# Optimization experiments

Measured on AMD Instinct MI355X. Metric: run time of the kernel, lower is better.

## Reference

```python
import jax, jax.numpy as jnp
import numpy as np

N_NODES = 50000
N_EDGES = 500000
NEG_SLOPE = 0.2


def gat_layer(x, src, dst, W, a_src, a_dst, b, n):
    """PyG-style GATConv (add_self_loops=True, concat=True, eval mode).
    x: [N, F_in], W: [F_in, H*C], a_src/a_dst: [H, C], b: [H*C]."""
    H, C = a_src.shape
    h = (x @ W).reshape(-1, H, C)              # [N, H, C]
    loops = jnp.arange(n, dtype=src.dtype)
    s = jnp.concatenate([src, loops])          # self-loops appended
    d = jnp.concatenate([dst, loops])
    alpha_src = jnp.einsum('nhc,hc->nh', h, a_src)   # [N, H]
    alpha_dst = jnp.einsum('nhc,hc->nh', h, a_dst)
    e = jax.nn.leaky_relu(alpha_src[s] + alpha_dst[d], NEG_SLOPE)  # [E+N, H]
    m = jax.ops.segment_max(e, d, num_segments=n)    # segment softmax over dst
    w = jnp.exp(e - m[d])
    denom = jax.ops.segment_sum(w, d, num_segments=n)
    attn = w / (denom[d] + 1e-16)                    # [E+N, H]
    msg = h[s] * attn[:, :, None]                    # [E+N, H, C]
    out = jax.ops.segment_sum(msg, d, num_segments=n)  # [N, H, C]
    return out.reshape(n, H * C) + b


def setup_inputs() -> dict:
    key = jax.random.key(0)
    ks = jax.random.split(key, 20)
    F_in, Hd, Hh = 128, 64, 4
    g = lambda k, shp, fan: jax.random.normal(k, shp, jnp.float32) * (1.0 / np.sqrt(fan))
    inp = {
        'x': jax.random.normal(ks[0], (N_NODES, F_in), jnp.float32),
        'edge_index': jax.random.randint(ks[1], (2, N_EDGES), 0, N_NODES, jnp.int32),
        'W1': g(ks[2], (F_in, Hh * Hd), F_in),
        'a1s': g(ks[3], (Hh, Hd), Hd), 'a1d': g(ks[4], (Hh, Hd), Hd),
        'b1': jnp.zeros((Hh * Hd,), jnp.float32),
        'W2': g(ks[5], (Hh * Hd, Hh * Hd), Hh * Hd),
        'a2s': g(ks[6], (Hh, Hd), Hd), 'a2d': g(ks[7], (Hh, Hd), Hd),
        'b2': jnp.zeros((Hh * Hd,), jnp.float32),
        'W3': g(ks[8], (Hh * Hd, Hd), Hh * Hd),
        'a3s': g(ks[9], (1, Hd), Hd), 'a3d': g(ks[10], (1, Hd), Hd),
        'b3': jnp.zeros((Hd,), jnp.float32),
        'cW1': g(ks[11], (Hd, Hd // 2), Hd), 'cb1': jnp.zeros((Hd // 2,), jnp.float32),
        'cW2': g(ks[12], (Hd // 2, 2), Hd // 2), 'cb2': jnp.zeros((2,), jnp.float32),
    }
    return inp


def reference(x, edge_index, W1, a1s, a1d, b1, W2, a2s, a2d, b2,
              W3, a3s, a3d, b3, cW1, cb1, cW2, cb2):
    n = x.shape[0]
    src, dst = edge_index[0], edge_index[1]
    h = jax.nn.elu(gat_layer(x, src, dst, W1, a1s, a1d, b1, n))
    h = jax.nn.elu(gat_layer(h, src, dst, W2, a2s, a2d, b2, n))
    h = jax.nn.relu(gat_layer(h, src, dst, W3, a3s, a3d, b3, n))
    h = jax.nn.relu(h @ cW1 + cb1)
    logits = h @ cW2 + cb2
    return jax.nn.log_softmax(logits, axis=1)
```

## Files before the change

### kernel.cpp

```cpp
#include <hip/hip_runtime.h>
#include <hip/hip_fp16.h>

#define LRELU(v) ((v) > 0.f ? (v) : 0.2f * (v))

typedef _Float16 f16x8 __attribute__((ext_vector_type(8)));
typedef float f32x4 __attribute__((ext_vector_type(4)));

__device__ __forceinline__ f16x8 f16x8_zero() {
    f16x8 v;
#pragma unroll
    for (int j = 0; j < 8; ++j) v[j] = (_Float16)0.f;
    return v;
}

__global__ __launch_bounds__(256) void hist_kernel(const int* __restrict__ dst,
                                                   int* __restrict__ cnt, int E) {
    int e = blockIdx.x * 256 + threadIdx.x;
    if (e < E) atomicAdd(&cnt[dst[e]], 1);
}

__global__ __launch_bounds__(256) void scan_blk(const int* __restrict__ cnt,
                                                int* __restrict__ offv,
                                                int* __restrict__ bsum, int N) {
    __shared__ int sh[256];
    const int t = threadIdx.x;
    const int base = blockIdx.x * 1024 + t * 4;
    int v0 = (base + 0 < N) ? cnt[base + 0] : 0;
    int v1 = (base + 1 < N) ? cnt[base + 1] : 0;
    int v2 = (base + 2 < N) ? cnt[base + 2] : 0;
    int v3 = (base + 3 < N) ? cnt[base + 3] : 0;
    const int T = v0 + v1 + v2 + v3;
    sh[t] = T;
    __syncthreads();
    for (int o = 1; o < 256; o <<= 1) {
        int x = (t >= o) ? sh[t - o] : 0;
        __syncthreads();
        sh[t] += x;
        __syncthreads();
    }
    const int excl = sh[t] - T;
    if (t == 255) bsum[blockIdx.x] = sh[255];
    if (base + 0 < N) offv[base + 0] = excl;
    if (base + 1 < N) offv[base + 1] = excl + v0;
    if (base + 2 < N) offv[base + 2] = excl + v0 + v1;
    if (base + 3 < N) offv[base + 3] = excl + v0 + v1 + v2;
}

__global__ __launch_bounds__(64) void scan_top(int* __restrict__ bsum,
                                               int* __restrict__ offv,
                                               int NB, int N) {
    const int t = threadIdx.x;
    const int v = (t < NB) ? bsum[t] : 0;
    int incl = v;
#pragma unroll
    for (int o = 1; o < 64; o <<= 1) {
        int x = __shfl_up(incl, o);
        if (t >= o) incl += x;
    }
    if (t < NB) bsum[t] = incl - v;
    if (t == NB - 1) offv[N] = incl;
}

__global__ __launch_bounds__(256) void scan_add(int* __restrict__ offv,
                                                const int* __restrict__ bsum, int N) {
    const int base = blockIdx.x * 1024 + threadIdx.x * 4;
    const int add = bsum[blockIdx.x];
#pragma unroll
    for (int i = 0; i < 4; ++i)
        if (base + i < N) offv[base + i] += add;
}

__global__ __launch_bounds__(256) void fill_kernel(const int* __restrict__ dst,
                                                   const int* __restrict__ srcv,
                                                   const int* __restrict__ offv,
                                                   int* __restrict__ cur,
                                                   int* __restrict__ csrsrc, int E) {
    int e = blockIdx.x * 256 + threadIdx.x;
    if (e < E) {
        int d = dst[e];
        int p = atomicAdd(&cur[d], 1);
        csrsrc[offv[d] + p] = srcv[e];
    }
}

__global__ __launch_bounds__(256) void prep_w16(const float* __restrict__ W,
                                                _Float16* __restrict__ wt,
                                                int K, int Nn) {
    int idx = blockIdx.x * 256 + threadIdx.x;
    if (idx < K * Nn) {
        int k = idx / Nn, nn2 = idx - k * Nn;
        wt[(size_t)nn2 * K + k] = (_Float16)W[idx];
    }
}

__global__ __launch_bounds__(256) void cvt_f16(const float* __restrict__ in,
                                               _Float16* __restrict__ out, int n4) {
    int i = blockIdx.x * 256 + threadIdx.x;
    if (i < n4) {
        float4 v = *(const float4*)(in + (size_t)i * 4);
        _Float16 o[4] = {(_Float16)v.x, (_Float16)v.y, (_Float16)v.z, (_Float16)v.w};
        *(float2*)(out + (size_t)i * 4) = *(float2*)o;
    }
}

template <int WM, int WN, int K, int H>
__global__ __launch_bounds__(WM * WN * 64) void gemm_f16_fused(
    const _Float16* __restrict__ A, const _Float16* __restrict__ Wt,
    const float* __restrict__ a_s, const float* __restrict__ a_d,
    _Float16* __restrict__ hout, float* __restrict__ als,
    float* __restrict__ ald, int M, int Nn) {
    constexpr int BM = WM * 64;
    constexpr int T = WM * WN * 64;
    constexpr int CHUNKS = BM * 16;
    __shared__ f16x8 Atile[BM * 16];
    const int t = threadIdx.x;
    const int lane = t & 63;
    const int wv = t >> 6;
    const int wm = wv / WN, wn = wv % WN;
    const int m0 = blockIdx.x * BM;
    const int n0 = blockIdx.y * (WN * 64);
    const int l15 = lane & 15, lg = lane >> 4;

    f32x4 acc[4][4];
    const f32x4 zz = {0.f, 0.f, 0.f, 0.f};
#pragma unroll
    for (int mi = 0; mi < 4; ++mi)
#pragma unroll
        for (int ni = 0; ni < 4; ++ni) acc[mi][ni] = zz;

    for (int kc = 0; kc < K; kc += 128) {
        __syncthreads();
#pragma unroll
        for (int i = 0; i < CHUNKS / T; ++i) {
            const int c = i * T + t;
            const int row = c >> 4, cc = c & 15;
            const int gr = m0 + row;
            f16x8 v = (gr < M) ? *(const f16x8*)(A + (size_t)gr * K + kc + cc * 8)
                               : f16x8_zero();
            Atile[(row * 16 + cc) ^ (row & 7)] = v;
        }
        __syncthreads();
#pragma unroll
        for (int ks = 0; ks < 4; ++ks) {
            f16x8 af[4], bf[4];
#pragma unroll
            for (int mi = 0; mi < 4; ++mi) {
                const int row = wm * 64 + mi * 16 + l15;
                af[mi] = Atile[(row * 16 + ks * 4 + lg) ^ (row & 7)];
            }
#pragma unroll
            for (int ni = 0; ni < 4; ++ni) {
                const int col = n0 + wn * 64 + ni * 16 + l15;
                bf[ni] = *(const f16x8*)(Wt + (size_t)col * K + kc + ks * 32 + lg * 8);
            }
#pragma unroll
            for (int mi = 0; mi < 4; ++mi)
#pragma unroll
                for (int ni = 0; ni < 4; ++ni)
                    acc[mi][ni] = __builtin_amdgcn_mfma_f32_16x16x32_f16(
                        af[mi], bf[ni], acc[mi][ni], 0, 0, 0);
        }
    }
    const int head = (n0 + wn * 64) >> 6;
    float a4s[4], a4d[4];
#pragma unroll
    for (int ni = 0; ni < 4; ++ni) {
        a4s[ni] = a_s[head * 64 + ni * 16 + l15];
        a4d[ni] = a_d[head * 64 + ni * 16 + l15];
    }
#pragma unroll
    for (int mi = 0; mi < 4; ++mi)
#pragma unroll
        for (int j = 0; j < 4; ++j) {
            const int r = m0 + wm * 64 + mi * 16 + lg * 4 + j;
            if (r < M) {
                float s1 = 0.f, s2 = 0.f;
#pragma unroll
                for (int ni = 0; ni < 4; ++ni) {
                    const float v = acc[mi][ni][j];
                    s1 += v * a4s[ni];
                    s2 += v * a4d[ni];
                    hout[(size_t)r * Nn + n0 + wn * 64 + ni * 16 + l15] = (_Float16)v;
                }
#pragma unroll
                for (int o = 8; o; o >>= 1) {
                    s1 += __shfl_xor(s1, o);
                    s2 += __shfl_xor(s2, o);
                }
                if (l15 == 0) {
                    als[(size_t)r * H + head] = s1;
                    ald[(size_t)r * H + head] = s2;
                }
            }
        }
}

__device__ __forceinline__ float sel4(float4 v, int h) {
    float r = v.x;
    r = (h == 1) ? v.y : r;
    r = (h == 2) ? v.z : r;
    r = (h == 3) ? v.w : r;
    return r;
}

__global__ __launch_bounds__(64) void gat_agg_h4(
    const __half* __restrict__ hhf, const float4* __restrict__ als4,
    const float4* __restrict__ ald4, const int* __restrict__ csrsrc,
    const int* __restrict__ offv, const float* __restrict__ bias,
    __half* __restrict__ outh) {
    const int n = blockIdx.x;
    const int t = threadIdx.x;
    const int hh = t >> 4;
    __shared__ int sid[64];
    __shared__ float4 wsh[64];
    const int start = offv[n];
    const int deg = offv[n + 1] - start;
    const float4 ad = ald4[n];
    const float4 asf = als4[n];
    float4 ws4;
    ws4.x = __expf(LRELU(asf.x + ad.x));
    ws4.y = __expf(LRELU(asf.y + ad.y));
    ws4.z = __expf(LRELU(asf.z + ad.z));
    ws4.w = __expf(LRELU(asf.w + ad.w));
    const float wself = sel4(ws4, hh);
    float acc[4];
    {
        float2 raw = *(const float2*)(hhf + (size_t)n * 256 + t * 4);
        __half2 h0 = *(__half2*)&raw.x;
        __half2 h1 = *(__half2*)&raw.y;
        float2 a0 = __half22float2(h0), a1 = __half22float2(h1);
        acc[0] = a0.x * wself; acc[1] = a0.y * wself;
        acc[2] = a1.x * wself; acc[3] = a1.y * wself;
    }
    float dsum = wself;

    for (int base = 0; base < deg; base += 64) {
        const int nb = deg - base;
        int s = 0;
        float4 w4 = {0.f, 0.f, 0.f, 0.f};
        if (t < nb) {
            s = csrsrc[start + base + t];
            const float4 av = als4[s];
            w4.x = __expf(LRELU(av.x + ad.x));
            w4.y = __expf(LRELU(av.y + ad.y));
            w4.z = __expf(LRELU(av.z + ad.z));
            w4.w = __expf(LRELU(av.w + ad.w));
        }
        __syncthreads();
        sid[t] = s;
        wsh[t] = w4;
        __syncthreads();
        const int nbc = min(nb, 64);
        const float* wflat = (const float*)wsh;
        for (int i = 0; i < nbc; ++i) {
            const int s2 = sid[i];
            const float wvv = wflat[i * 4 + hh];
            float2 raw = *(const float2*)(hhf + (size_t)s2 * 256 + t * 4);
            __half2 h0 = *(__half2*)&raw.x;
            __half2 h1 = *(__half2*)&raw.y;
            float2 a0 = __half22float2(h0), a1 = __half22float2(h1);
            dsum += wvv;
            acc[0] += a0.x * wvv; acc[1] += a0.y * wvv;
            acc[2] += a1.x * wvv; acc[3] += a1.y * wvv;
        }
    }
    const float inv = 1.f / (dsum + 1e-16f);
    const float4 bv = *(const float4*)(bias + t * 4);
    float4 o4;
    o4.x = acc[0] * inv + bv.x;
    o4.y = acc[1] * inv + bv.y;
    o4.z = acc[2] * inv + bv.z;
    o4.w = acc[3] * inv + bv.w;
    o4.x = (o4.x > 0.f) ? o4.x : (__expf(o4.x) - 1.f);
    o4.y = (o4.y > 0.f) ? o4.y : (__expf(o4.y) - 1.f);
    o4.z = (o4.z > 0.f) ? o4.z : (__expf(o4.z) - 1.f);
    o4.w = (o4.w > 0.f) ? o4.w : (__expf(o4.w) - 1.f);
    __half2 p0 = __floats2half2_rn(o4.x, o4.y);
    __half2 p1 = __floats2half2_rn(o4.z, o4.w);
    float2 st;
    *(__half2*)&st.x = p0;
    *(__half2*)&st.y = p1;
    *(float2*)(outh + (size_t)n * 256 + t * 4) = st;
}

__global__ __launch_bounds__(64) void gat_agg_h1_cls(
    const __half* __restrict__ hhf, const float* __restrict__ als,
    const float* __restrict__ ald, const int* __restrict__ csrsrc,
    const int* __restrict__ offv, const float* __restrict__ bias,
    const float* __restrict__ cW1, const float* __restrict__ cb1,
    const float* __restrict__ cW2, const float* __restrict__ cb2,
    float* __restrict__ outp) {
    const int n = blockIdx.x;
    const int t = threadIdx.x;
    __shared__ int sid[64];
    __shared__ float wsh[64];
    __shared__ float xs[64];
    __shared__ float hid[32];
    __shared__ float lg[2];
    const int start = offv[n];
    const int deg = offv[n + 1] - start;
    const float ad = ald[n];
    const float wself = __expf(LRELU(als[n] + ad));
    float acc = __half2float(hhf[(size_t)n * 64 + t]) * wself;
    float dsum = wself;

    for (int base = 0; base < deg; base += 64) {
        const int nb = deg - base;
        int s = 0;
        float w = 0.f;
        if (t < nb) {
            s = csrsrc[start + base + t];
            w = __expf(LRELU(als[s] + ad));
        }
        __syncthreads();
        sid[t] = s;
        wsh[t] = w;
        __syncthreads();
        const int nbc = min(nb, 64);
        for (int i = 0; i < nbc; ++i) {
            const float wvv = wsh[i];
            dsum += wvv;
            acc += __half2float(hhf[(size_t)sid[i] * 64 + t]) * wvv;
        }
    }
    float val = acc / (dsum + 1e-16f) + bias[t];
    val = fmaxf(val, 0.f);
    __syncthreads();
    xs[t] = val;
    __syncthreads();
    if (t < 32) {
        float s = cb1[t];
#pragma unroll
        for (int c = 0; c < 64; ++c) s += xs[c] * cW1[c * 32 + t];
        hid[t] = fmaxf(s, 0.f);
    }
    __syncthreads();
    if (t < 2) {
        float s = cb2[t];
#pragma unroll
        for (int j = 0; j < 32; ++j) s += hid[j] * cW2[j * 2 + t];
        lg[t] = s;
    }
    __syncthreads();
    if (t == 0) {
        float a = lg[0], b = lg[1];
        float mm = fmaxf(a, b);
        float lse = mm + logf(__expf(a - mm) + __expf(b - mm));
        outp[(size_t)n * 2 + 0] = a - lse;
        outp[(size_t)n * 2 + 1] = b - lse;
    }
}

extern "C" void kernel_launch(void* const* d_in, const int* in_sizes, int n_in,
                              void* d_out, int out_size, void* d_ws, size_t ws_size,
                              hipStream_t stream) {
    const float* x   = (const float*)d_in[0];
    const int*   ei  = (const int*)d_in[1];
    const float* W1  = (const float*)d_in[2];
    const float* a1s = (const float*)d_in[3];
    const float* a1d = (const float*)d_in[4];
    const float* b1  = (const float*)d_in[5];
    const float* W2  = (const float*)d_in[6];
    const float* a2s = (const float*)d_in[7];
    const float* a2d = (const float*)d_in[8];
    const float* b2  = (const float*)d_in[9];
    const float* W3  = (const float*)d_in[10];
    const float* a3s = (const float*)d_in[11];
    const float* a3d = (const float*)d_in[12];
    const float* b3  = (const float*)d_in[13];
    const float* cW1 = (const float*)d_in[14];
    const float* cb1 = (const float*)d_in[15];
    const float* cW2 = (const float*)d_in[16];
    const float* cb2 = (const float*)d_in[17];

    const int N = in_sizes[0] / 128;
    const int E = in_sizes[1] / 2;
    const int* srcv = ei;
    const int* dstv = ei + E;

    char* p = (char*)d_ws;
    _Float16* slotA = (_Float16*)p; p += (size_t)N * 256 * 2;
    _Float16* slotB = (_Float16*)p; p += (size_t)N * 256 * 2;
    _Float16* slotC = (_Float16*)p; p += (size_t)N * 128 * 2;
    float* als = (float*)p; p += (size_t)N * 4 * 4;
    float* ald = (float*)p; p += (size_t)N * 4 * 4;
    int* cnt = (int*)p; p += (size_t)N * 4;
    int* offv = (int*)p; p += (size_t)(N + 4) * 4;
    int* csr = (int*)p; p += (size_t)E * 4;
    _Float16* Wt1 = (_Float16*)p; p += (size_t)128 * 256 * 2;
    _Float16* Wt2 = (_Float16*)p; p += (size_t)256 * 256 * 2;
    _Float16* Wt3 = (_Float16*)p; p += (size_t)256 * 64 * 2;
    int* bsum = (int*)p;

    prep_w16<<<(128 * 256 + 255) / 256, 256, 0, stream>>>(W1, Wt1, 128, 256);
    prep_w16<<<(256 * 256 + 255) / 256, 256, 0, stream>>>(W2, Wt2, 256, 256);
    prep_w16<<<(256 * 64 + 255) / 256, 256, 0, stream>>>(W3, Wt3, 256, 64);
    cvt_f16<<<(N * 128 / 4 + 255) / 256, 256, 0, stream>>>(x, slotC, N * 128 / 4);

    const int NB = (N + 1023) / 1024;
    hipMemsetAsync(cnt, 0, (size_t)N * sizeof(int), stream);
    hist_kernel<<<(E + 255) / 256, 256, 0, stream>>>(dstv, cnt, E);
    scan_blk<<<NB, 256, 0, stream>>>(cnt, offv, bsum, N);
    scan_top<<<1, 64, 0, stream>>>(bsum, offv, NB, N);
    scan_add<<<NB, 256, 0, stream>>>(offv, bsum, N);
    hipMemsetAsync(cnt, 0, (size_t)N * sizeof(int), stream);
    fill_kernel<<<(E + 255) / 256, 256, 0, stream>>>(dstv, srcv, offv, cnt, csr, E);

    const int MB128 = (N + 127) / 128;
    const int MB256 = (N + 255) / 256;

    gemm_f16_fused<2, 4, 128, 4><<<dim3(MB128, 1), 512, 0, stream>>>(
        slotC, Wt1, a1s, a1d, slotA, als, ald, N, 256);
    gat_agg_h4<<<N, 64, 0, stream>>>((const __half*)slotA, (const float4*)als,
                                     (const float4*)ald, csr, offv, b1,
                                     (__half*)slotB);

    gemm_f16_fused<2, 4, 256, 4><<<dim3(MB128, 1), 512, 0, stream>>>(
        slotB, Wt2, a2s, a2d, slotA, als, ald, N, 256);
    gat_agg_h4<<<N, 64, 0, stream>>>((const __half*)slotA, (const float4*)als,
                                     (const float4*)ald, csr, offv, b2,
                                     (__half*)slotB);

    gemm_f16_fused<4, 1, 256, 1><<<dim3(MB256, 1), 256, 0, stream>>>(
        slotB, Wt3, a3s, a3d, slotA, als, ald, N, 64);
    gat_agg_h1_cls<<<N, 64, 0, stream>>>((const __half*)slotA, als, ald, csr, offv,
                                         b3, cW1, cb1, cW2, cb2, (float*)d_out);
}
```

Measured before the change: 296.0 us.

## Replace shared-memory staging with wave shuffles and pack four nodes per block

The aggregation kernels now process one destination node per 64-lane wavefront, with four nodes per 256-thread block. Edge indices and attention weights are broadcast with __shfl instead of being staged in LDS behind __syncthreads. The classifier head also uses shuffles rather than shared memory. In the 4-head kernel each 16-lane group computes its own head's weights for batches of 16 edges, which removes the per-block barriers and the tiny 64-thread blocks but means four times as many edge-batch iterations.

```diff
diff --git a/kernel.cpp b/kernel.cpp
--- a/kernel.cpp
+++ b/kernel.cpp
@@ -195,34 +195,20 @@
         }
 }
 
-__device__ __forceinline__ float sel4(float4 v, int h) {
-    float r = v.x;
-    r = (h == 1) ? v.y : r;
-    r = (h == 2) ? v.z : r;
-    r = (h == 3) ? v.w : r;
-    return r;
-}
-
-__global__ __launch_bounds__(64) void gat_agg_h4(
-    const __half* __restrict__ hhf, const float4* __restrict__ als4,
-    const float4* __restrict__ ald4, const int* __restrict__ csrsrc,
+
+__global__ __launch_bounds__(256) void gat_agg_h4(
+    const __half* __restrict__ hhf, const float* __restrict__ als,
+    const float* __restrict__ ald, const int* __restrict__ csrsrc,
     const int* __restrict__ offv, const float* __restrict__ bias,
-    __half* __restrict__ outh) {
-    const int n = blockIdx.x;
-    const int t = threadIdx.x;
-    const int hh = t >> 4;
-    __shared__ int sid[64];
-    __shared__ float4 wsh[64];
+    __half* __restrict__ outh, int N) {
+    const int t = threadIdx.x & 63;
+    const int n = blockIdx.x * 4 + (threadIdx.x >> 6);
+    if (n >= N) return;
+    const int eidx = t & 15, head = t >> 4, lbase = t & 48;
     const int start = offv[n];
     const int deg = offv[n + 1] - start;
-    const float4 ad = ald4[n];
-    const float4 asf = als4[n];
-    float4 ws4;
-    ws4.x = __expf(LRELU(asf.x + ad.x));
-    ws4.y = __expf(LRELU(asf.y + ad.y));
-    ws4.z = __expf(LRELU(asf.z + ad.z));
-    ws4.w = __expf(LRELU(asf.w + ad.w));
-    const float wself = sel4(ws4, hh);
+    const float adh = ald[n * 4 + head];
+    const float wself = __expf(LRELU(als[n * 4 + head] + adh));
     float acc[4];
     {
         float2 raw = *(const float2*)(hhf + (size_t)n * 256 + t * 4);
@@ -234,34 +220,25 @@
     }
     float dsum = wself;
 
-    for (int base = 0; base < deg; base += 64) {
-        const int nb = deg - base;
+    for (int base = 0; base < deg; base += 16) {
+        const int nb = min(16, deg - base);
         int s = 0;
-        float4 w4 = {0.f, 0.f, 0.f, 0.f};
-        if (t < nb) {
-            s = csrsrc[start + base + t];
-            const float4 av = als4[s];
-            w4.x = __expf(LRELU(av.x + ad.x));
-            w4.y = __expf(LRELU(av.y + ad.y));
-            w4.z = __expf(LRELU(av.z + ad.z));
-            w4.w = __expf(LRELU(av.w + ad.w));
-        }
-        __syncthreads();
-        sid[t] = s;
-        wsh[t] = w4;
-        __syncthreads();
-        const int nbc = min(nb, 64);
-        const float* wflat = (const float*)wsh;
-        for (int i = 0; i < nbc; ++i) {
-            const int s2 = sid[i];
-            const float wvv = wflat[i * 4 + hh];
-            float2 raw = *(const float2*)(hhf + (size_t)s2 * 256 + t * 4);
+        float w = 0.f;
+        if (eidx < nb) {
+            s = csrsrc[start + base + eidx];
+            w = __expf(LRELU(als[s * 4 + head] + adh));
+        }
+#pragma unroll 4
+        for (int i = 0; i < nb; ++i) {
+            const int si = __shfl(s, lbase | i);
+            const float wi = __shfl(w, lbase | i);
+            float2 raw = *(const float2*)(hhf + (size_t)si * 256 + t * 4);
             __half2 h0 = *(__half2*)&raw.x;
             __half2 h1 = *(__half2*)&raw.y;
             float2 a0 = __half22float2(h0), a1 = __half22float2(h1);
-            dsum += wvv;
-            acc[0] += a0.x * wvv; acc[1] += a0.y * wvv;
-            acc[2] += a1.x * wvv; acc[3] += a1.y * wvv;
+            dsum += wi;
+            acc[0] += a0.x * wi; acc[1] += a0.y * wi;
+            acc[2] += a1.x * wi; acc[3] += a1.y * wi;
         }
     }
     const float inv = 1.f / (dsum + 1e-16f);
@@ -283,20 +260,16 @@
     *(float2*)(outh + (size_t)n * 256 + t * 4) = st;
 }
 
-__global__ __launch_bounds__(64) void gat_agg_h1_cls(
+__global__ __launch_bounds__(256) void gat_agg_h1_cls(
     const __half* __restrict__ hhf, const float* __restrict__ als,
     const float* __restrict__ ald, const int* __restrict__ csrsrc,
     const int* __restrict__ offv, const float* __restrict__ bias,
     const float* __restrict__ cW1, const float* __restrict__ cb1,
     const float* __restrict__ cW2, const float* __restrict__ cb2,
-    float* __restrict__ outp) {
-    const int n = blockIdx.x;
-    const int t = threadIdx.x;
-    __shared__ int sid[64];
-    __shared__ float wsh[64];
-    __shared__ float xs[64];
-    __shared__ float hid[32];
-    __shared__ float lg[2];
+    float* __restrict__ outp, int N) {
+    const int t = threadIdx.x & 63;
+    const int n = blockIdx.x * 4 + (threadIdx.x >> 6);
+    if (n >= N) return;
     const int start = offv[n];
     const int deg = offv[n + 1] - start;
     const float ad = ald[n];
@@ -312,43 +285,34 @@
             s = csrsrc[start + base + t];
             w = __expf(LRELU(als[s] + ad));
         }
-        __syncthreads();
-        sid[t] = s;
-        wsh[t] = w;
-        __syncthreads();
         const int nbc = min(nb, 64);
+#pragma unroll 4
         for (int i = 0; i < nbc; ++i) {
-            const float wvv = wsh[i];
-            dsum += wvv;
-            acc += __half2float(hhf[(size_t)sid[i] * 64 + t]) * wvv;
-        }
-    }
-    float val = acc / (dsum + 1e-16f) + bias[t];
-    val = fmaxf(val, 0.f);
-    __syncthreads();
-    xs[t] = val;
-    __syncthreads();
-    if (t < 32) {
-        float s = cb1[t];
-#pragma unroll
-        for (int c = 0; c < 64; ++c) s += xs[c] * cW1[c * 32 + t];
-        hid[t] = fmaxf(s, 0.f);
-    }
-    __syncthreads();
-    if (t < 2) {
-        float s = cb2[t];
-#pragma unroll
-        for (int j = 0; j < 32; ++j) s += hid[j] * cW2[j * 2 + t];
-        lg[t] = s;
-    }
-    __syncthreads();
-    if (t == 0) {
-        float a = lg[0], b = lg[1];
-        float mm = fmaxf(a, b);
-        float lse = mm + logf(__expf(a - mm) + __expf(b - mm));
-        outp[(size_t)n * 2 + 0] = a - lse;
-        outp[(size_t)n * 2 + 1] = b - lse;
-    }
+            const int si = __shfl(s, i);
+            const float wi = __shfl(w, i);
+            dsum += wi;
+            acc += __half2float(hhf[(size_t)si * 64 + t]) * wi;
+        }
+    }
+    const float val = fmaxf(acc / (dsum + 1e-16f) + bias[t], 0.f);
+    float s1 = cb1[t & 31];
+#pragma unroll
+    for (int c = 0; c < 64; ++c) {
+        const float xv = __shfl(val, c);
+        s1 += xv * cW1[c * 32 + (t & 31)];
+    }
+    const float hidv = fmaxf(s1, 0.f);
+    float s2 = cb2[t & 1];
+#pragma unroll
+    for (int j = 0; j < 32; ++j) {
+        const float hj = __shfl(hidv, j);
+        s2 += hj * cW2[j * 2 + (t & 1)];
+    }
+    const float a = __shfl(s2, 0);
+    const float b = __shfl(s2, 1);
+    const float mm = fmaxf(a, b);
+    const float lse = mm + logf(__expf(a - mm) + __expf(b - mm));
+    if (t < 2) outp[(size_t)n * 2 + t] = s2 - lse;
 }
 
 extern "C" void kernel_launch(void* const* d_in, const int* in_sizes, int n_in,
@@ -408,21 +372,21 @@
 
     const int MB128 = (N + 127) / 128;
     const int MB256 = (N + 255) / 256;
+    const int AGG = (N + 3) / 4;
 
     gemm_f16_fused<2, 4, 128, 4><<<dim3(MB128, 1), 512, 0, stream>>>(
         slotC, Wt1, a1s, a1d, slotA, als, ald, N, 256);
-    gat_agg_h4<<<N, 64, 0, stream>>>((const __half*)slotA, (const float4*)als,
-                                     (const float4*)ald, csr, offv, b1,
-                                     (__half*)slotB);
+    gat_agg_h4<<<AGG, 256, 0, stream>>>((const __half*)slotA, als, ald, csr, offv,
+                                        b1, (__half*)slotB, N);
 
     gemm_f16_fused<2, 4, 256, 4><<<dim3(MB128, 1), 512, 0, stream>>>(
         slotB, Wt2, a2s, a2d, slotA, als, ald, N, 256);
-    gat_agg_h4<<<N, 64, 0, stream>>>((const __half*)slotA, (const float4*)als,
-                                     (const float4*)ald, csr, offv, b2,
-                                     (__half*)slotB);
+    gat_agg_h4<<<AGG, 256, 0, stream>>>((const __half*)slotA, als, ald, csr, offv,
+                                        b2, (__half*)slotB, N);
 
     gemm_f16_fused<4, 1, 256, 1><<<dim3(MB256, 1), 256, 0, stream>>>(
         slotB, Wt3, a3s, a3d, slotA, als, ald, N, 64);
-    gat_agg_h1_cls<<<N, 64, 0, stream>>>((const __half*)slotA, als, ald, csr, offv,
-                                         b3, cW1, cb1, cW2, cb2, (float*)d_out);
-}
+    gat_agg_h1_cls<<<AGG, 256, 0, stream>>>((const __half*)slotA, als, ald, csr,
+                                            offv, b3, cW1, cb1, cW2, cb2,
+                                            (float*)d_out, N);
+}
```

After: 328.2 us. +10.9%, slower.
